# Performance work log

Measured on AMD Instinct MI355X. Metric: run time of the kernel, lower is better.

Reference implementation:

```python
import jax, jax.numpy as jnp
import numpy as np
from jax import lax

MAX_OBJ = 100
IOU_THRES = 0.45
SCORE_THRES = 0.25
MAX_WH = 7680.0

# xywh -> xyxy conversion matrix (same as ONNX_ORT.convert_matrix)
CONVERT = jnp.array([[1, 0, 1, 0],
                     [0, 1, 0, 1],
                     [-0.5, 0, 0.5, 0],
                     [0, -0.5, 0, 0.5]], dtype=jnp.float32)


def _iou_one_vs_all(box, boxes):
    # box: [4] xyxy, boxes: [N,4] xyxy
    x1 = jnp.maximum(box[0], boxes[:, 0])
    y1 = jnp.maximum(box[1], boxes[:, 1])
    x2 = jnp.minimum(box[2], boxes[:, 2])
    y2 = jnp.minimum(box[3], boxes[:, 3])
    inter = jnp.clip(x2 - x1, 0.0) * jnp.clip(y2 - y1, 0.0)
    a = (box[2] - box[0]) * (box[3] - box[1])
    b = (boxes[:, 2] - boxes[:, 0]) * (boxes[:, 3] - boxes[:, 1])
    return inter / (a + b - inter + 1e-9)


def _nms_indices(nmsbox, max_score):
    # Greedy class-offset NMS; returns [MAX_OBJ] indices, -1 for padding.
    valid0 = max_score >= SCORE_THRES

    def step(valid, _):
        s = jnp.where(valid, max_score, -1.0)
        i = jnp.argmax(s)
        ok = s[i] >= SCORE_THRES
        iou = _iou_one_vs_all(nmsbox[i], nmsbox)
        valid = valid & (iou <= IOU_THRES)
        valid = valid.at[i].set(False)
        return valid, jnp.where(ok, i, -1)

    _, idxs = lax.scan(step, valid0, None, length=MAX_OBJ)
    return idxs


def _forward(x1, x2, num_labels1, num_labels2):
    B, N1, _ = x1.shape
    N2 = x2.shape[1]
    # pad x1 class scores with zeros for model2's labels (appended at end)
    x1p = jnp.concatenate([x1, jnp.zeros((B, N1, num_labels2), x1.dtype)], axis=2)
    # pad x2: insert zeros for model1's labels between conf and its own classes
    x2p = jnp.concatenate([x2[:, :, 0:5],
                           jnp.zeros((B, N2, num_labels1), x2.dtype),
                           x2[:, :, 5:]], axis=2)
    x = jnp.concatenate([x1p, x2p], axis=1)  # [B, N1+N2, 5+C1+C2]

    boxes = x[:, :, :4] @ CONVERT            # xywh -> xyxy, [B,N,4]
    conf = x[:, :, 4:5]
    scores = x[:, :, 5:] * conf              # [B,N,C]
    max_score = scores.max(axis=2)           # [B,N]
    cat_id = scores.argmax(axis=2)           # [B,N]
    # class-offset boxes so NMS is class-aware
    nmsbox = boxes + cat_id[..., None].astype(boxes.dtype) * MAX_WH

    idxs = jax.vmap(_nms_indices)(lax.stop_gradient(nmsbox),
                                  lax.stop_gradient(max_score))  # [B,MAX_OBJ]
    mask = idxs >= 0
    si = jnp.maximum(idxs, 0)
    sel_boxes = jnp.take_along_axis(boxes, si[..., None], axis=1)      # [B,MAX_OBJ,4]
    sel_cat = jnp.take_along_axis(cat_id, si, axis=1).astype(boxes.dtype)
    sel_score = jnp.take_along_axis(max_score, si, axis=1)

    mf = mask.astype(boxes.dtype)
    Xcol = jnp.where(mask, jnp.arange(B)[:, None], -1).astype(boxes.dtype)
    out = jnp.concatenate([Xcol[..., None],
                           sel_boxes * mf[..., None],
                           (sel_cat * mf)[..., None],
                           (sel_score * mf)[..., None]], axis=2)
    return out.reshape(B * MAX_OBJ, 7)


def setup_inputs() -> dict:
    key = jax.random.key(0)
    k1, k2 = jax.random.split(key)
    x1 = jax.random.uniform(k1, (4, 25200, 85), dtype=jnp.float32)
    x2 = jax.random.uniform(k2, (4, 25200, 25), dtype=jnp.float32)
    return {"x1": x1, "x2": x2, "num_labels1": 80, "num_labels2": 20}


def reference(x1, x2, num_labels1, num_labels2):
    return _forward(x1, x2, num_labels1, num_labels2)
```

## Files before the change

### kernel.cpp

```cpp
#include <hip/hip_runtime.h>
#include <stdint.h>

#pragma clang fp contract(off)

#define BATCH 4
#define N1 25200
#define NROW 50400
#define NCLS 100
#define TOT (BATCH*NROW)
#define CAPB 2048
#define CAPG 1152
#define SCORE_T 0.25f
#define IOU_T 0.45f
#define MAXWH 7680.0f

#define X1_SLAB 64
#define X1_SPB 394
#define X2_SLAB 256
#define X2_SPB 99

typedef unsigned long long u64;

__device__ __forceinline__ u64 pack_key(unsigned sb, int n, int cid) {
    return ((u64)sb << 32) | ((u64)(unsigned)((n ^ 0xFFFF) & 0xFFFF) << 8) | (u64)(unsigned)cid;
}

__device__ __forceinline__ bool sup_test(float inter, float sum) {
    float d = (sum - inter) + 1e-9f;
    float t1 = IOU_T * d;
    bool hi = inter > t1 * 1.00001f;
    bool lo = inter < t1 * 0.99999f;
    if (__builtin_expect(!(hi || lo), 0)) return (inter / d) > IOU_T;
    return hi;
}

__device__ __forceinline__ float rl(float v, int srcLane) {
    return __int_as_float(__builtin_amdgcn_readlane(__float_as_int(v), srcLane));
}

__device__ __forceinline__ void blk2bucket(int blk, int& b, int& c) {
    if (blk < BATCH * 20) { b = blk / 20; c = 80 + (blk - b * 20); }
    else { int z = blk - BATCH * 20; b = z / 80; c = z - b * 80; }
}

__global__ __launch_bounds__(256) void k_rows(const float* __restrict__ x1,
                                              const float* __restrict__ x2,
                                              float4* __restrict__ boxes4,
                                              u64* __restrict__ rowKey) {
    __shared__ float4 ld4[1600];
    float* ld = (float*)ld4;
    int blk = blockIdx.x;
    int t = threadIdx.x;
    const int NX1 = BATCH * X1_SPB;
    if (blk < NX1) {
        int b = blk / X1_SPB, s = blk - b * X1_SPB;
        int r0 = s * X1_SLAB;
        int nr = min(X1_SLAB, N1 - r0);
        const float4* src = (const float4*)(x1 + ((size_t)b * N1 + r0) * 85);
        int count4 = (nr * 85) >> 2;
        for (int i = t; i < count4; i += 256) ld4[i] = src[i];
        __syncthreads();
        int row = t >> 2, sub = t & 3;
        if (row < nr) {
            const float* p = ld + row * 85;
            float conf = p[4];
            u64 key = 0ULL;
            int base = sub * 20;
            for (int c = 0; c < 20; ++c) {
                int j = base + c;
                float v = p[5 + j] * conf;
                u64 kk = ((u64)__float_as_uint(v) << 32) | (unsigned)~(unsigned)j;
                if (kk > key) key = kk;
            }
            u64 o;
            o = __shfl_xor(key, 1, 64); if (o > key) key = o;
            o = __shfl_xor(key, 2, 64); if (o > key) key = o;
            if (sub == 0) {
                float best = __uint_as_float((unsigned)(key >> 32));
                int bestj = ~(unsigned)key;
                int n = r0 + row;
                int r = b * NROW + n;
                u64 outk = 0ULL;
                if (best >= SCORE_T) {
                    float cx = p[0], cy = p[1], w = p[2], h = p[3];
                    boxes4[r] = make_float4(cx - 0.5f * w, cy - 0.5f * h,
                                            cx + 0.5f * w, cy + 0.5f * h);
                    outk = pack_key((unsigned)(key >> 32), n, bestj);
                }
                rowKey[r] = outk;
            }
        }
    } else {
        int blk2 = blk - NX1;
        int b = blk2 / X2_SPB, s = blk2 - b * X2_SPB;
        int r0 = s * X2_SLAB;
        int nr = min(X2_SLAB, N1 - r0);
        const float4* src = (const float4*)(x2 + ((size_t)b * N1 + r0) * 25);
        int count4 = (nr * 25) >> 2;
        for (int i = t; i < count4; i += 256) ld4[i] = src[i];
        __syncthreads();
        if (t < nr) {
            const float* p = ld + t * 25;
            float conf = p[4];
            float best = 0.0f; int bestj = 0;
            for (int j2 = 0; j2 < 20; ++j2) {
                float v = p[5 + j2] * conf;
                if (v > best) { best = v; bestj = 80 + j2; }
            }
            int n = N1 + r0 + t;
            int r = b * NROW + n;
            u64 outk = 0ULL;
            if (best >= SCORE_T) {
                float cx = p[0], cy = p[1], w = p[2], h = p[3];
                boxes4[r] = make_float4(cx - 0.5f * w, cy - 0.5f * h,
                                        cx + 0.5f * w, cy + 0.5f * h);
                outk = pack_key(__float_as_uint(best), n, bestj);
            }
            rowKey[r] = outk;
        }
    }
}

__global__ __launch_bounds__(256) void k_prep(const u64* __restrict__ rowKey,
                                              u64* __restrict__ skG,
                                              int* __restrict__ cntArr) {
    __shared__ u64 sk[CAPB];
    __shared__ u64 temp2[2048];
    __shared__ int wcnt[4];
    int b, c; blk2bucket(blockIdx.x, b, c);
    int bucket = b * NCLS + c;
    int t = threadIdx.x;
    int lane = t & 63, wid = t >> 6;

    int rowBase = (c >= 80) ? N1 : 0;
    const ulonglong2* rk2 = (const ulonglong2*)(rowKey + (size_t)b * NROW + rowBase);
    const int SLICE = 3150;
    u64* temp = temp2 + wid * 512;
    int wbase = 0;
    for (int i = wid * SLICE + lane; i < (wid + 1) * SLICE; i += 64) {
        ulonglong2 kk = rk2[i];
        bool m0 = (kk.x != 0ULL) && ((int)(kk.x & 0xFF) == c);
        bool m1 = (kk.y != 0ULL) && ((int)(kk.y & 0xFF) == c);
        u64 mb0 = __ballot(m0), mb1 = __ballot(m1);
        u64 below = (1ULL << lane) - 1ULL;
        if (m0) { int p = wbase + __popcll(mb0 & below); if (p < 512) temp[p] = kk.x; }
        if (m1) { int p = wbase + __popcll(mb0) + __popcll(mb1 & below); if (p < 512) temp[p] = kk.y; }
        wbase += __popcll(mb0) + __popcll(mb1);
    }
    if (lane == 0) wcnt[wid] = min(wbase, 512);
    __syncthreads();
    int w0 = wcnt[0], w1 = wcnt[1], w2 = wcnt[2], w3 = wcnt[3];
    int cnt0 = w0 + w1 + w2 + w3;
    if (cnt0 == 0) { if (t == 0) cntArr[bucket] = 0; return; }
    int myoff = (wid > 0 ? w0 : 0) + (wid > 1 ? w1 : 0) + (wid > 2 ? w2 : 0);
    int mycnt = wcnt[wid];
    for (int i = lane; i < mycnt; i += 64) sk[myoff + i] = temp[i];
    int L = 512; while (L < cnt0) L <<= 1;
    for (int i = cnt0 + t; i < L; i += 256) sk[i] = 0ULL;
    __syncthreads();

    bool act = (t * 8) < L;
    u64 r[8];
    if (act) {
#pragma unroll
        for (int e = 0; e < 8; ++e) r[e] = sk[t * 8 + e];
    }
    for (int k = 2; k <= L; k <<= 1) {
        for (int j = k >> 1; j > 0; j >>= 1) {
            if (j >= 512) {
                if (act) {
#pragma unroll
                    for (int e = 0; e < 8; ++e) sk[t * 8 + e] = r[e];
                }
                __syncthreads();
                if (act) {
                    bool iAmLo = (t & (j >> 3)) == 0;
                    bool descSeg = (t & (k >> 3)) == 0;
                    bool takeMax = (descSeg == iAmLo);
#pragma unroll
                    for (int e = 0; e < 8; ++e) {
                        u64 u = r[e];
                        u64 v = sk[(t * 8 + e) ^ j];
                        bool uGE = (u >= v);
                        r[e] = (takeMax == uGE) ? u : v;
                    }
                }
                __syncthreads();
            } else if (j >= 8) {
                if (act) {
                    int dt = j >> 3;
                    bool iAmLo = (t & dt) == 0;
                    bool descSeg = (t & (k >> 3)) == 0;
                    bool takeMax = (descSeg == iAmLo);
#pragma unroll
                    for (int e = 0; e < 8; ++e) {
                        u64 u = r[e];
                        u64 v = __shfl_xor(u, dt, 64);
                        bool uGE = (u >= v);
                        r[e] = (takeMax == uGE) ? u : v;
                    }
                }
            } else {
                if (act) {
#pragma unroll
                    for (int e = 0; e < 8; ++e) {
                        if (!(e & j)) {
                            int e2 = e | j;
                            bool descSeg = (k >= 8) ? ((t & (k >> 3)) == 0)
                                                    : ((e & k) == 0);
                            u64 lo = r[e], hi = r[e2];
                            bool sw = descSeg ? (lo < hi) : (lo > hi);
                            if (sw) { r[e] = hi; r[e2] = lo; }
                        }
                    }
                }
            }
        }
    }
    if (act) {
#pragma unroll
        for (int e = 0; e < 8; ++e) sk[t * 8 + e] = r[e];
    }
    __syncthreads();

    int cw = min(cnt0, CAPG);
    for (int i = t; i < cw; i += 256) skG[(size_t)bucket * CAPG + i] = sk[i];
    if (t == 0) cntArr[bucket] = cw;
}

__global__ __launch_bounds__(64) void k_greedy(const float4* __restrict__ boxes4,
                                               const u64* __restrict__ skG,
                                               const int* __restrict__ cntArr,
                                               u64* __restrict__ accKey,
                                               int* __restrict__ accCnt) {
    __shared__ float4 accQ[100];
    __shared__ float accA[100];
    int b, c; blk2bucket(blockIdx.x, b, c);
    int bucket = b * NCLS + c;
    int lane = threadIdx.x;
    int cnt0 = cntArr[bucket];
    if (cnt0 == 0) { if (lane == 0) accCnt[bucket] = 0; return; }
    const u64* skB = skG + (size_t)bucket * CAPG;
    float off = (float)c * MAXWH;
    int m = 0;
    for (int base = 0; base < cnt0 && m < 100; base += 64) {
        int j = base + lane;
        bool alive = (j < cnt0);
        float4 a = make_float4(0.f, 0.f, 0.f, 0.f);
        float aA = 0.f; u64 myKey = 0ULL;
        if (alive) {
            myKey = skB[j];
            int n = 0xFFFF ^ (int)((myKey >> 8) & 0xFFFF);
            a = boxes4[b * NROW + n];
            a.x += off; a.y += off; a.z += off; a.w += off;
            aA = (a.z - a.x) * (a.w - a.y);
        }
        int k2 = 0;
        while (k2 < m) {
            if (__ballot(alive) == 0ULL) break;
            int rem = m - k2;
            if (rem >= 8) {
#pragma unroll
                for (int u = 0; u < 8; ++u) {
                    float4 q = accQ[k2 + u];
                    float qa = accA[k2 + u];
                    float xx1 = fmaxf(a.x, q.x), yy1 = fmaxf(a.y, q.y);
                    float xx2 = fminf(a.z, q.z), yy2 = fminf(a.w, q.w);
                    float inter = fmaxf(xx2 - xx1, 0.f) * fmaxf(yy2 - yy1, 0.f);
                    alive = alive && !sup_test(inter, qa + aA);
                }
                k2 += 8;
            } else {
                for (int u = 0; u < rem; ++u) {
                    float4 q = accQ[k2 + u];
                    float qa = accA[k2 + u];
                    float xx1 = fmaxf(a.x, q.x), yy1 = fmaxf(a.y, q.y);
                    float xx2 = fminf(a.z, q.z), yy2 = fminf(a.w, q.w);
                    float inter = fmaxf(xx2 - xx1, 0.f) * fmaxf(yy2 - yy1, 0.f);
                    alive = alive && !sup_test(inter, qa + aA);
                }
                k2 = m;
            }
        }
        u64 av = __ballot(alive);
        while (av != 0ULL && m < 100) {
            int f = __builtin_ctzll(av);
            float qx = rl(a.x, f), qy = rl(a.y, f);
            float qz = rl(a.z, f), qw = rl(a.w, f);
            float qa = rl(aA, f);
            if (lane == f) {
                accQ[m] = a; accA[m] = aA;
                accKey[(size_t)bucket * 100 + m] = myKey;
                alive = false;
            }
            ++m;
            if (alive) {
                float xx1 = fmaxf(a.x, qx), yy1 = fmaxf(a.y, qy);
                float xx2 = fminf(a.z, qz), yy2 = fminf(a.w, qw);
                float inter = fmaxf(xx2 - xx1, 0.f) * fmaxf(yy2 - yy1, 0.f);
                alive = !sup_test(inter, qa + aA);
            }
            av = __ballot(alive);
        }
    }
    if (lane == 0) accCnt[bucket] = m;
}

__global__ __launch_bounds__(256) void k_merge(const float4* __restrict__ boxes4,
                                               const u64* __restrict__ accKey,
                                               const int* __restrict__ accCnt,
                                               float* __restrict__ out) {
    __shared__ u64 keys[NCLS * 100];
    __shared__ u64 winKey[100];
    __shared__ int cnts[NCLS];
    int b = blockIdx.x;
    int t = threadIdx.x;
    if (t < NCLS) cnts[t] = accCnt[b * NCLS + t];
    __syncthreads();
    for (int i = t; i < NCLS * 100; i += 256) {
        int c = i / 100, j = i - c * 100;
        keys[i] = (j < cnts[c]) ? accKey[(size_t)(b * NCLS + c) * 100 + j] : 0ULL;
    }
    __syncthreads();
    if (t < 64) {
        int c0 = 2 * t, c1 = 2 * t + 1;
        int h0 = 0, h1 = 0;
        u64 hk0 = (c0 < NCLS && cnts[c0] > 0) ? keys[c0 * 100] : 0ULL;
        u64 hk1 = (c1 < NCLS && cnts[c1] > 0) ? keys[c1 * 100] : 0ULL;
        for (int step = 0; step < 100; ++step) {
            u64 k = (hk0 >= hk1) ? hk0 : hk1;
            for (int o = 1; o < 64; o <<= 1) {
                u64 ok = __shfl_xor(k, o, 64);
                if (ok > k) k = ok;
            }
            if (t == 0) winKey[step] = k;
            if (k != 0ULL) {
                int cls = (int)(k & 0xFF);
                if (cls == c0)      { ++h0; hk0 = (h0 < cnts[c0]) ? keys[c0 * 100 + h0] : 0ULL; }
                else if (cls == c1) { ++h1; hk1 = (h1 < cnts[c1]) ? keys[c1 * 100 + h1] : 0ULL; }
            }
        }
    }
    __syncthreads();
    if (t < 100) {
        u64 k = winKey[t];
        float* o7 = out + (size_t)(b * 100 + t) * 7;
        if (k == 0ULL) {
            o7[0] = -1.0f;
            o7[1] = 0.0f; o7[2] = 0.0f; o7[3] = 0.0f;
            o7[4] = 0.0f; o7[5] = 0.0f; o7[6] = 0.0f;
        } else {
            int n = 0xFFFF ^ (int)((k >> 8) & 0xFFFF);
            int cid = (int)(k & 0xFF);
            float4 bx = boxes4[b * NROW + n];
            o7[0] = (float)b;
            o7[1] = bx.x; o7[2] = bx.y; o7[3] = bx.z; o7[4] = bx.w;
            o7[5] = (float)cid;
            o7[6] = __uint_as_float((unsigned)(k >> 32));
        }
    }
}

extern "C" void kernel_launch(void* const* d_in, const int* in_sizes, int n_in,
                              void* d_out, int out_size, void* d_ws, size_t ws_size,
                              hipStream_t stream) {
    const float* x1 = (const float*)d_in[0];
    const float* x2 = (const float*)d_in[1];
    float* out = (float*)d_out;

    float4* boxes4 = (float4*)d_ws;
    u64* rowKey = (u64*)(boxes4 + TOT);
    u64* skG    = rowKey + TOT;
    u64* accKey = skG + (size_t)BATCH * NCLS * CAPG;
    int* cntArr = (int*)(accKey + (size_t)BATCH * NCLS * 100);
    int* accCnt = cntArr + BATCH * NCLS;

    int rowBlocks = BATCH * X1_SPB + BATCH * X2_SPB;
    k_rows<<<rowBlocks, 256, 0, stream>>>(x1, x2, boxes4, rowKey);
    k_prep<<<BATCH * NCLS, 256, 0, stream>>>(rowKey, skG, cntArr);
    k_greedy<<<BATCH * NCLS, 64, 0, stream>>>(boxes4, skG, cntArr, accKey, accCnt);
    k_merge<<<BATCH, 256, 0, stream>>>(boxes4, accKey, accCnt, out);
}
```

Baseline: 166.1 us.

## Replace serial 100-step merge with threshold select plus bitonic sort

The merge kernel previously picked the top 100 keys from 100 per-class sorted lists with a serial 100-step single-wave tournament. It now binary-searches a key threshold that leaves between 100 and 900 candidates, compacts those into shared memory with ballot and atomics, and bitonic-sorts 1024 keys with the full block. The sort is factored into a shared helper reused by the bucket kernel. This trades a long serial dependency chain for up to 64 parallel counting passes with block syncs.

```diff
diff --git a/kernel.cpp b/kernel.cpp
--- a/kernel.cpp
+++ b/kernel.cpp
@@ -41,6 +41,72 @@
 __device__ __forceinline__ void blk2bucket(int blk, int& b, int& c) {
     if (blk < BATCH * 20) { b = blk / 20; c = 80 + (blk - b * 20); }
     else { int z = blk - BATCH * 20; b = z / 80; c = z - b * 80; }
+}
+
+__device__ __forceinline__ void sort_desc(u64* sk, int L, int t) {
+    bool act = (t * 8) < L;
+    u64 r[8];
+    if (act) {
+#pragma unroll
+        for (int e = 0; e < 8; ++e) r[e] = sk[t * 8 + e];
+    }
+    for (int k = 2; k <= L; k <<= 1) {
+        for (int j = k >> 1; j > 0; j >>= 1) {
+            if (j >= 512) {
+                if (act) {
+#pragma unroll
+                    for (int e = 0; e < 8; ++e) sk[t * 8 + e] = r[e];
+                }
+                __syncthreads();
+                if (act) {
+                    bool iAmLo = (t & (j >> 3)) == 0;
+                    bool descSeg = (t & (k >> 3)) == 0;
+                    bool takeMax = (descSeg == iAmLo);
+#pragma unroll
+                    for (int e = 0; e < 8; ++e) {
+                        u64 u = r[e];
+                        u64 v = sk[(t * 8 + e) ^ j];
+                        bool uGE = (u >= v);
+                        r[e] = (takeMax == uGE) ? u : v;
+                    }
+                }
+                __syncthreads();
+            } else if (j >= 8) {
+                if (act) {
+                    int dt = j >> 3;
+                    bool iAmLo = (t & dt) == 0;
+                    bool descSeg = (t & (k >> 3)) == 0;
+                    bool takeMax = (descSeg == iAmLo);
+#pragma unroll
+                    for (int e = 0; e < 8; ++e) {
+                        u64 u = r[e];
+                        u64 v = __shfl_xor(u, dt, 64);
+                        bool uGE = (u >= v);
+                        r[e] = (takeMax == uGE) ? u : v;
+                    }
+                }
+            } else {
+                if (act) {
+#pragma unroll
+                    for (int e = 0; e < 8; ++e) {
+                        if (!(e & j)) {
+                            int e2 = e | j;
+                            bool descSeg = (k >= 8) ? ((t & (k >> 3)) == 0)
+                                                    : ((e & k) == 0);
+                            u64 lo = r[e], hi = r[e2];
+                            bool sw = descSeg ? (lo < hi) : (lo > hi);
+                            if (sw) { r[e] = hi; r[e2] = lo; }
+                        }
+                    }
+                }
+            }
+        }
+    }
+    if (act) {
+#pragma unroll
+        for (int e = 0; e < 8; ++e) sk[t * 8 + e] = r[e];
+    }
+    __syncthreads();
 }
 
 __global__ __launch_bounds__(256) void k_rows(const float* __restrict__ x1,
@@ -159,69 +225,7 @@
     for (int i = cnt0 + t; i < L; i += 256) sk[i] = 0ULL;
     __syncthreads();
 
-    bool act = (t * 8) < L;
-    u64 r[8];
-    if (act) {
-#pragma unroll
-        for (int e = 0; e < 8; ++e) r[e] = sk[t * 8 + e];
-    }
-    for (int k = 2; k <= L; k <<= 1) {
-        for (int j = k >> 1; j > 0; j >>= 1) {
-            if (j >= 512) {
-                if (act) {
-#pragma unroll
-                    for (int e = 0; e < 8; ++e) sk[t * 8 + e] = r[e];
-                }
-                __syncthreads();
-                if (act) {
-                    bool iAmLo = (t & (j >> 3)) == 0;
-                    bool descSeg = (t & (k >> 3)) == 0;
-                    bool takeMax = (descSeg == iAmLo);
-#pragma unroll
-                    for (int e = 0; e < 8; ++e) {
-                        u64 u = r[e];
-                        u64 v = sk[(t * 8 + e) ^ j];
-                        bool uGE = (u >= v);
-                        r[e] = (takeMax == uGE) ? u : v;
-                    }
-                }
-                __syncthreads();
-            } else if (j >= 8) {
-                if (act) {
-                    int dt = j >> 3;
-                    bool iAmLo = (t & dt) == 0;
-                    bool descSeg = (t & (k >> 3)) == 0;
-                    bool takeMax = (descSeg == iAmLo);
-#pragma unroll
-                    for (int e = 0; e < 8; ++e) {
-                        u64 u = r[e];
-                        u64 v = __shfl_xor(u, dt, 64);
-                        bool uGE = (u >= v);
-                        r[e] = (takeMax == uGE) ? u : v;
-                    }
-                }
-            } else {
-                if (act) {
-#pragma unroll
-                    for (int e = 0; e < 8; ++e) {
-                        if (!(e & j)) {
-                            int e2 = e | j;
-                            bool descSeg = (k >= 8) ? ((t & (k >> 3)) == 0)
-                                                    : ((e & k) == 0);
-                            u64 lo = r[e], hi = r[e2];
-                            bool sw = descSeg ? (lo < hi) : (lo > hi);
-                            if (sw) { r[e] = hi; r[e2] = lo; }
-                        }
-                    }
-                }
-            }
-        }
-    }
-    if (act) {
-#pragma unroll
-        for (int e = 0; e < 8; ++e) sk[t * 8 + e] = r[e];
-    }
-    __syncthreads();
+    sort_desc(sk, L, t);
 
     int cw = min(cnt0, CAPG);
     for (int i = t; i < cw; i += 256) skG[(size_t)bucket * CAPG + i] = sk[i];
@@ -311,39 +315,60 @@
                                                const int* __restrict__ accCnt,
                                                float* __restrict__ out) {
     __shared__ u64 keys[NCLS * 100];
-    __shared__ u64 winKey[100];
+    __shared__ u64 sk[1024];
     __shared__ int cnts[NCLS];
-    int b = blockIdx.x;
-    int t = threadIdx.x;
+    __shared__ int red[4];
+    __shared__ int gcnt;
+    int b = blockIdx.x, t = threadIdx.x;
+    int lane = t & 63, wid = t >> 6;
     if (t < NCLS) cnts[t] = accCnt[b * NCLS + t];
+    if (t == 0) gcnt = 0;
     __syncthreads();
     for (int i = t; i < NCLS * 100; i += 256) {
         int c = i / 100, j = i - c * 100;
         keys[i] = (j < cnts[c]) ? accKey[(size_t)(b * NCLS + c) * 100 + j] : 0ULL;
     }
     __syncthreads();
-    if (t < 64) {
-        int c0 = 2 * t, c1 = 2 * t + 1;
-        int h0 = 0, h1 = 0;
-        u64 hk0 = (c0 < NCLS && cnts[c0] > 0) ? keys[c0 * 100] : 0ULL;
-        u64 hk1 = (c1 < NCLS && cnts[c1] > 0) ? keys[c1 * 100] : 0ULL;
-        for (int step = 0; step < 100; ++step) {
-            u64 k = (hk0 >= hk1) ? hk0 : hk1;
-            for (int o = 1; o < 64; o <<= 1) {
-                u64 ok = __shfl_xor(k, o, 64);
-                if (ok > k) k = ok;
-            }
-            if (t == 0) winKey[step] = k;
-            if (k != 0ULL) {
-                int cls = (int)(k & 0xFF);
-                if (cls == c0)      { ++h0; hk0 = (h0 < cnts[c0]) ? keys[c0 * 100 + h0] : 0ULL; }
-                else if (cls == c1) { ++h1; hk1 = (h1 < cnts[c1]) ? keys[c1 * 100 + h1] : 0ULL; }
-            }
-        }
-    }
-    __syncthreads();
+    int S = 0;
+    for (int c = 0; c < NCLS; ++c) S += cnts[c];
+    u64 T = 0ULL;
+    if (S > 900) {
+        u64 lo = 0ULL, hi = ~0ULL;
+        for (int it = 0; it < 64; ++it) {
+            u64 mid = lo + ((hi - lo) >> 1);
+            int cl = 0;
+            for (int i = t; i < NCLS * 100; i += 256) cl += (keys[i] > mid) ? 1 : 0;
+            for (int o = 1; o < 64; o <<= 1) cl += __shfl_xor(cl, o, 64);
+            if (lane == 0) red[wid] = cl;
+            __syncthreads();
+            int cnt = red[0] + red[1] + red[2] + red[3];
+            __syncthreads();
+            if (cnt >= 100 && cnt <= 900) { T = mid; break; }
+            if (cnt < 100) hi = mid; else lo = mid;
+            T = lo;
+        }
+    }
+    for (int i = t; i < NCLS * 100; i += 256) {
+        u64 k = keys[i];
+        bool take = (k > T);
+        u64 mb = __ballot(take);
+        if (mb != 0ULL) {
+            int basew;
+            if (lane == 0) basew = atomicAdd(&gcnt, __popcll(mb));
+            basew = __shfl(basew, 0, 64);
+            if (take) {
+                int p = basew + __popcll(mb & ((1ULL << lane) - 1ULL));
+                if (p < 1024) sk[p] = k;
+            }
+        }
+    }
+    __syncthreads();
+    int G = min(gcnt, 1024);
+    for (int i = G + t; i < 1024; i += 256) sk[i] = 0ULL;
+    __syncthreads();
+    sort_desc(sk, 1024, t);
     if (t < 100) {
-        u64 k = winKey[t];
+        u64 k = sk[t];
         float* o7 = out + (size_t)(b * 100 + t) * 7;
         if (k == 0ULL) {
             o7[0] = -1.0f;
```

Result: slower. 186.5 us (+12.3%).

## Replace serial per-batch k-way merge with parallel rank-by-binary-search scatter

Applied to the files above, without the earlier changes.

The final merge, which ran on only 4 blocks doing 100 serial wavefront-wide max reductions over 100 sorted class lists, is replaced by 400 blocks. In each, every accepted key finds its global rank by binary-searching all class lists and writes its output row directly when the rank is below 100. Padding rows are now pre-filled with the -1/0 pattern in k_prep so unfilled slots stay correct. The sort body is moved into a helper function without behaviour change. This trades a serial dependency chain for more global-memory reads in the binary searches and relies on all keys being unique to produce distinct ranks.

```diff
diff --git a/kernel.cpp b/kernel.cpp
--- a/kernel.cpp
+++ b/kernel.cpp
@@ -41,6 +41,72 @@
 __device__ __forceinline__ void blk2bucket(int blk, int& b, int& c) {
     if (blk < BATCH * 20) { b = blk / 20; c = 80 + (blk - b * 20); }
     else { int z = blk - BATCH * 20; b = z / 80; c = z - b * 80; }
+}
+
+__device__ __forceinline__ void sort_desc(u64* sk, int L, int t) {
+    bool act = (t * 8) < L;
+    u64 r[8];
+    if (act) {
+#pragma unroll
+        for (int e = 0; e < 8; ++e) r[e] = sk[t * 8 + e];
+    }
+    for (int k = 2; k <= L; k <<= 1) {
+        for (int j = k >> 1; j > 0; j >>= 1) {
+            if (j >= 512) {
+                if (act) {
+#pragma unroll
+                    for (int e = 0; e < 8; ++e) sk[t * 8 + e] = r[e];
+                }
+                __syncthreads();
+                if (act) {
+                    bool iAmLo = (t & (j >> 3)) == 0;
+                    bool descSeg = (t & (k >> 3)) == 0;
+                    bool takeMax = (descSeg == iAmLo);
+#pragma unroll
+                    for (int e = 0; e < 8; ++e) {
+                        u64 u = r[e];
+                        u64 v = sk[(t * 8 + e) ^ j];
+                        bool uGE = (u >= v);
+                        r[e] = (takeMax == uGE) ? u : v;
+                    }
+                }
+                __syncthreads();
+            } else if (j >= 8) {
+                if (act) {
+                    int dt = j >> 3;
+                    bool iAmLo = (t & dt) == 0;
+                    bool descSeg = (t & (k >> 3)) == 0;
+                    bool takeMax = (descSeg == iAmLo);
+#pragma unroll
+                    for (int e = 0; e < 8; ++e) {
+                        u64 u = r[e];
+                        u64 v = __shfl_xor(u, dt, 64);
+                        bool uGE = (u >= v);
+                        r[e] = (takeMax == uGE) ? u : v;
+                    }
+                }
+            } else {
+                if (act) {
+#pragma unroll
+                    for (int e = 0; e < 8; ++e) {
+                        if (!(e & j)) {
+                            int e2 = e | j;
+                            bool descSeg = (k >= 8) ? ((t & (k >> 3)) == 0)
+                                                    : ((e & k) == 0);
+                            u64 lo = r[e], hi = r[e2];
+                            bool sw = descSeg ? (lo < hi) : (lo > hi);
+                            if (sw) { r[e] = hi; r[e2] = lo; }
+                        }
+                    }
+                }
+            }
+        }
+    }
+    if (act) {
+#pragma unroll
+        for (int e = 0; e < 8; ++e) sk[t * 8 + e] = r[e];
+    }
+    __syncthreads();
 }
 
 __global__ __launch_bounds__(256) void k_rows(const float* __restrict__ x1,
@@ -123,7 +189,8 @@
 
 __global__ __launch_bounds__(256) void k_prep(const u64* __restrict__ rowKey,
                                               u64* __restrict__ skG,
-                                              int* __restrict__ cntArr) {
+                                              int* __restrict__ cntArr,
+                                              float* __restrict__ out) {
     __shared__ u64 sk[CAPB];
     __shared__ u64 temp2[2048];
     __shared__ int wcnt[4];
@@ -131,6 +198,11 @@
     int bucket = b * NCLS + c;
     int t = threadIdx.x;
     int lane = t & 63, wid = t >> 6;
+
+    if (blockIdx.x < BATCH) {
+        float* ob = out + (size_t)blockIdx.x * NCLS * 7;
+        for (int i = t; i < NCLS * 7; i += 256) ob[i] = (i % 7 == 0) ? -1.0f : 0.0f;
+    }
 
     int rowBase = (c >= 80) ? N1 : 0;
     const ulonglong2* rk2 = (const ulonglong2*)(rowKey + (size_t)b * NROW + rowBase);
@@ -159,69 +231,7 @@
     for (int i = cnt0 + t; i < L; i += 256) sk[i] = 0ULL;
     __syncthreads();
 
-    bool act = (t * 8) < L;
-    u64 r[8];
-    if (act) {
-#pragma unroll
-        for (int e = 0; e < 8; ++e) r[e] = sk[t * 8 + e];
-    }
-    for (int k = 2; k <= L; k <<= 1) {
-        for (int j = k >> 1; j > 0; j >>= 1) {
-            if (j >= 512) {
-                if (act) {
-#pragma unroll
-                    for (int e = 0; e < 8; ++e) sk[t * 8 + e] = r[e];
-                }
-                __syncthreads();
-                if (act) {
-                    bool iAmLo = (t & (j >> 3)) == 0;
-                    bool descSeg = (t & (k >> 3)) == 0;
-                    bool takeMax = (descSeg == iAmLo);
-#pragma unroll
-                    for (int e = 0; e < 8; ++e) {
-                        u64 u = r[e];
-                        u64 v = sk[(t * 8 + e) ^ j];
-                        bool uGE = (u >= v);
-                        r[e] = (takeMax == uGE) ? u : v;
-                    }
-                }
-                __syncthreads();
-            } else if (j >= 8) {
-                if (act) {
-                    int dt = j >> 3;
-                    bool iAmLo = (t & dt) == 0;
-                    bool descSeg = (t & (k >> 3)) == 0;
-                    bool takeMax = (descSeg == iAmLo);
-#pragma unroll
-                    for (int e = 0; e < 8; ++e) {
-                        u64 u = r[e];
-                        u64 v = __shfl_xor(u, dt, 64);
-                        bool uGE = (u >= v);
-                        r[e] = (takeMax == uGE) ? u : v;
-                    }
-                }
-            } else {
-                if (act) {
-#pragma unroll
-                    for (int e = 0; e < 8; ++e) {
-                        if (!(e & j)) {
-                            int e2 = e | j;
-                            bool descSeg = (k >= 8) ? ((t & (k >> 3)) == 0)
-                                                    : ((e & k) == 0);
-                            u64 lo = r[e], hi = r[e2];
-                            bool sw = descSeg ? (lo < hi) : (lo > hi);
-                            if (sw) { r[e] = hi; r[e2] = lo; }
-                        }
-                    }
-                }
-            }
-        }
-    }
-    if (act) {
-#pragma unroll
-        for (int e = 0; e < 8; ++e) sk[t * 8 + e] = r[e];
-    }
-    __syncthreads();
+    sort_desc(sk, L, t);
 
     int cw = min(cnt0, CAPG);
     for (int i = t; i < cw; i += 256) skG[(size_t)bucket * CAPG + i] = sk[i];
@@ -306,58 +316,51 @@
     if (lane == 0) accCnt[bucket] = m;
 }
 
-__global__ __launch_bounds__(256) void k_merge(const float4* __restrict__ boxes4,
-                                               const u64* __restrict__ accKey,
-                                               const int* __restrict__ accCnt,
-                                               float* __restrict__ out) {
-    __shared__ u64 keys[NCLS * 100];
-    __shared__ u64 winKey[100];
-    __shared__ int cnts[NCLS];
-    int b = blockIdx.x;
+__global__ __launch_bounds__(128) void k_rank(const float4* __restrict__ boxes4,
+                                              const u64* __restrict__ accKey,
+                                              const int* __restrict__ accCnt,
+                                              float* __restrict__ out) {
+    __shared__ int cnts[104];
+    int blk = blockIdx.x;
+    int b = blk / NCLS, c = blk - b * NCLS;
     int t = threadIdx.x;
-    if (t < NCLS) cnts[t] = accCnt[b * NCLS + t];
+    if (t < 104) cnts[t] = (t < NCLS) ? accCnt[b * NCLS + t] : 0;
     __syncthreads();
-    for (int i = t; i < NCLS * 100; i += 256) {
-        int c = i / 100, j = i - c * 100;
-        keys[i] = (j < cnts[c]) ? accKey[(size_t)(b * NCLS + c) * 100 + j] : 0ULL;
-    }
-    __syncthreads();
-    if (t < 64) {
-        int c0 = 2 * t, c1 = 2 * t + 1;
-        int h0 = 0, h1 = 0;
-        u64 hk0 = (c0 < NCLS && cnts[c0] > 0) ? keys[c0 * 100] : 0ULL;
-        u64 hk1 = (c1 < NCLS && cnts[c1] > 0) ? keys[c1 * 100] : 0ULL;
-        for (int step = 0; step < 100; ++step) {
-            u64 k = (hk0 >= hk1) ? hk0 : hk1;
-            for (int o = 1; o < 64; o <<= 1) {
-                u64 ok = __shfl_xor(k, o, 64);
-                if (ok > k) k = ok;
-            }
-            if (t == 0) winKey[step] = k;
-            if (k != 0ULL) {
-                int cls = (int)(k & 0xFF);
-                if (cls == c0)      { ++h0; hk0 = (h0 < cnts[c0]) ? keys[c0 * 100 + h0] : 0ULL; }
-                else if (cls == c1) { ++h1; hk1 = (h1 < cnts[c1]) ? keys[c1 * 100 + h1] : 0ULL; }
-            }
-        }
-    }
-    __syncthreads();
-    if (t < 100) {
-        u64 k = winKey[t];
-        float* o7 = out + (size_t)(b * 100 + t) * 7;
-        if (k == 0ULL) {
-            o7[0] = -1.0f;
-            o7[1] = 0.0f; o7[2] = 0.0f; o7[3] = 0.0f;
-            o7[4] = 0.0f; o7[5] = 0.0f; o7[6] = 0.0f;
-        } else {
-            int n = 0xFFFF ^ (int)((k >> 8) & 0xFFFF);
-            int cid = (int)(k & 0xFF);
-            float4 bx = boxes4[b * NROW + n];
-            o7[0] = (float)b;
-            o7[1] = bx.x; o7[2] = bx.y; o7[3] = bx.z; o7[4] = bx.w;
-            o7[5] = (float)cid;
-            o7[6] = __uint_as_float((unsigned)(k >> 32));
-        }
+    int myCnt = cnts[c];
+    if (t >= myCnt) return;
+    const u64* base = accKey + (size_t)b * NCLS * 100;
+    u64 myKey = base[c * 100 + t];
+    int rank = 0;
+    for (int g = 0; g < 104; g += 8) {
+        int lo[8], hi[8];
+#pragma unroll
+        for (int u = 0; u < 8; ++u) { lo[u] = 0; hi[u] = cnts[g + u]; }
+#pragma unroll
+        for (int s = 0; s < 7; ++s) {
+            int mid[8]; u64 kv[8];
+#pragma unroll
+            for (int u = 0; u < 8; ++u) {
+                mid[u] = (lo[u] + hi[u]) >> 1;
+                kv[u] = (lo[u] < hi[u]) ? base[(g + u) * 100 + mid[u]] : 0ULL;
+            }
+#pragma unroll
+            for (int u = 0; u < 8; ++u) {
+                if (lo[u] < hi[u]) {
+                    if (kv[u] > myKey) lo[u] = mid[u] + 1; else hi[u] = mid[u];
+                }
+            }
+        }
+#pragma unroll
+        for (int u = 0; u < 8; ++u) rank += lo[u];
+    }
+    if (rank < 100) {
+        int n = 0xFFFF ^ (int)((myKey >> 8) & 0xFFFF);
+        float4 bx = boxes4[b * NROW + n];
+        float* o7 = out + (size_t)(b * 100 + rank) * 7;
+        o7[0] = (float)b;
+        o7[1] = bx.x; o7[2] = bx.y; o7[3] = bx.z; o7[4] = bx.w;
+        o7[5] = (float)c;
+        o7[6] = __uint_as_float((unsigned)(myKey >> 32));
     }
 }
 
@@ -377,7 +380,7 @@
 
     int rowBlocks = BATCH * X1_SPB + BATCH * X2_SPB;
     k_rows<<<rowBlocks, 256, 0, stream>>>(x1, x2, boxes4, rowKey);
-    k_prep<<<BATCH * NCLS, 256, 0, stream>>>(rowKey, skG, cntArr);
+    k_prep<<<BATCH * NCLS, 256, 0, stream>>>(rowKey, skG, cntArr, out);
     k_greedy<<<BATCH * NCLS, 64, 0, stream>>>(boxes4, skG, cntArr, accKey, accCnt);
-    k_merge<<<BATCH, 256, 0, stream>>>(boxes4, accKey, accCnt, out);
-}
+    k_rank<<<BATCH * NCLS, 128, 0, stream>>>(boxes4, accKey, accCnt, out);
+}
```

Measured after the change: 246.9 us. +48.6%, slower.
